# Kernel tuning notes

Measured on AMD Instinct MI355X. Metric: run time of the kernel, lower is better.

The kernel has to match this reference:

```python
import jax, jax.numpy as jnp
import numpy as np

WS = 8          # window size
NH = 8          # num heads
DIM = 256
HD = DIM // NH  # head dim = 32
SCALE = HD ** -0.5
EPS = 1e-5


def _rel_pos_index(ws):
    # deterministic int index buffer, same math as the torch __init__
    coords = jnp.stack(jnp.meshgrid(jnp.arange(ws), jnp.arange(ws), indexing='ij'))  # [2,ws,ws]
    cf = coords.reshape(2, -1)                     # [2, N]
    rel = cf[:, :, None] - cf[:, None, :]          # [2, N, N]
    return (rel[0] + ws - 1) * (2 * ws - 1) + (rel[1] + ws - 1)  # [N, N]


def _ln(h, g, b):
    m = jnp.mean(h, axis=-1, keepdims=True)
    v = jnp.mean((h - m) ** 2, axis=-1, keepdims=True)
    return (h - m) / jnp.sqrt(v + EPS) * g + b


def setup_inputs() -> dict:
    key = jax.random.key(0)
    ks = jax.random.split(key, 16)
    B_, N, D = 4096, WS * WS, DIM
    s = 0.02
    return {
        'x':      jax.random.normal(ks[0], (B_, N, D), jnp.float32),
        # enhanced qkv: Linear(D,2D) -> LN -> GELU -> Linear(2D,3D)
        'w_qkv1': jax.random.normal(ks[1], (D, 2 * D), jnp.float32) * s,
        'b_qkv1': jnp.zeros((2 * D,), jnp.float32),
        'g_qkv':  jnp.ones((2 * D,), jnp.float32),
        'be_qkv': jnp.zeros((2 * D,), jnp.float32),
        'w_qkv2': jax.random.normal(ks[2], (2 * D, 3 * D), jnp.float32) * s,
        'b_qkv2': jnp.zeros((3 * D,), jnp.float32),
        # relative position bias table [(2*WS-1)^2, NH]
        'rpb':    jax.random.normal(ks[3], ((2 * WS - 1) ** 2, NH), jnp.float32) * s,
        # enhanced proj: Linear(D,2D) -> LN -> GELU -> Linear(2D,D)
        'w_p1':   jax.random.normal(ks[4], (D, 2 * D), jnp.float32) * s,
        'b_p1':   jnp.zeros((2 * D,), jnp.float32),
        'g_p':    jnp.ones((2 * D,), jnp.float32),
        'be_p':   jnp.zeros((2 * D,), jnp.float32),
        'w_p2':   jax.random.normal(ks[5], (2 * D, D), jnp.float32) * s,
        'b_p2':   jnp.zeros((D,), jnp.float32),
    }


def reference(x, w_qkv1, b_qkv1, g_qkv, be_qkv, w_qkv2, b_qkv2, rpb,
              w_p1, b_p1, g_p, be_p, w_p2, b_p2):
    B_, N, C = x.shape
    # enhanced QKV chain: Linear -> LayerNorm -> GELU -> Linear
    h = jax.nn.gelu(_ln(x @ w_qkv1 + b_qkv1, g_qkv, be_qkv), approximate=False)
    qkv = h @ w_qkv2 + b_qkv2                              # [B_, N, 3C]
    qkv = qkv.reshape(B_, N, 3, NH, HD).transpose(2, 0, 3, 1, 4)  # [3, B_, H, N, hd]
    q, k, v = qkv[0], qkv[1], qkv[2]
    attn = jnp.einsum('bhnd,bhmd->bhnm', q * SCALE, k)     # [B_, H, N, N]
    idx = _rel_pos_index(WS)                                # [N, N] int
    bias = rpb[idx.reshape(-1)].reshape(N, N, NH).transpose(2, 0, 1)  # [H, N, N]
    attn = jax.nn.softmax(attn + bias[None], axis=-1)
    out = jnp.einsum('bhnm,bhmd->bhnd', attn, v)           # [B_, H, N, hd]
    out = out.transpose(0, 2, 1, 3).reshape(B_, N, C)
    # enhanced proj chain: Linear -> LayerNorm -> GELU -> Linear
    h = jax.nn.gelu(_ln(out @ w_p1 + b_p1, g_p, be_p), approximate=False)
    return h @ w_p2 + b_p2
```

## Files before the change

kernel.cpp:

```cpp
#include <hip/hip_runtime.h>


typedef __bf16 bf16_t;
typedef __bf16 bf16x8 __attribute__((ext_vector_type(8)));
typedef __bf16 bf16x4 __attribute__((ext_vector_type(4)));
typedef float f32x4 __attribute__((ext_vector_type(4)));

__device__ __forceinline__ f32x4 mfma16(bf16x8 a, bf16x8 b, f32x4 acc) {
  return __builtin_amdgcn_mfma_f32_16x16x32_bf16(a, b, acc, 0, 0, 0);
}

#define SWZ(row, byteoff) ((byteoff) ^ (((row) & 7) << 4))

__device__ __forceinline__ float gelu_f(float v) {
  float e = __expf(v * (1.59576912f + 0.07135482f * v * v));
  return v - v * __builtin_amdgcn_rcpf(1.0f + e);
}

__global__ void prep_kernel(const float* __restrict__ w1, const float* __restrict__ w2,
                            const float* __restrict__ wp1, const float* __restrict__ wp2,
                            const float* __restrict__ rpb,
                            bf16_t* __restrict__ w1t, bf16_t* __restrict__ w2t,
                            bf16_t* __restrict__ wp1t, bf16_t* __restrict__ wp2t,
                            float* __restrict__ bt) {
  int i = blockIdx.x * 256 + threadIdx.x;
  if (i < 131072) {
    int k = i & 255, n = i >> 8;
    w1t[i] = (bf16_t)w1[k * 512 + n];
    return;
  }
  i -= 131072;
  if (i < 393216) {
    int k = i & 511, n = i >> 9;
    w2t[i] = (bf16_t)w2[k * 768 + n];
    return;
  }
  i -= 393216;
  if (i < 131072) {
    int k = i & 255, n = i >> 8;
    wp1t[i] = (bf16_t)wp1[k * 512 + n];
    return;
  }
  i -= 131072;
  if (i < 131072) {
    int k = i & 511, n = i >> 9;
    wp2t[i] = (bf16_t)wp2[k * 256 + n];
    return;
  }
  i -= 131072;
  if (i < 32768) {
    int hd = i >> 12, r = (i >> 6) & 63, j = i & 63;
    int idx = ((r >> 3) - (j >> 3) + 7) * 15 + ((r & 7) - (j & 7) + 7);
    bt[i] = rpb[idx * 8 + hd];
  }
}

__device__ __forceinline__ void gemmT_ln_gelu16(
    const char* bsrc, const bf16_t* __restrict__ wt,
    const float* __restrict__ bias, const float* __restrict__ gamma,
    const float* __restrict__ beta,
    char* dst, int flb, float2* part, int wave, int g, int c)
{
  f32x4 acc[2][4] = {};
#pragma unroll
  for (int kt = 0; kt < 8; ++kt) {
    bf16x8 a[2], b[4];
#pragma unroll
    for (int mt = 0; mt < 2; ++mt)
      a[mt] = *(const bf16x8*)(wt + (size_t)(wave * 32 + mt * 16 + c) * 256 + kt * 32 + g * 8);
#pragma unroll
    for (int nt = 0; nt < 4; ++nt) {
      int T = nt * 16 + c;
      b[nt] = *(const bf16x8*)(bsrc + SWZ(T, T * 512 + kt * 64 + g * 16));
    }
#pragma unroll
    for (int mt = 0; mt < 2; ++mt)
#pragma unroll
      for (int nt = 0; nt < 4; ++nt)
        acc[mt][nt] = mfma16(a[mt], b[nt], acc[mt][nt]);
  }
  float s[4] = {0.f, 0.f, 0.f, 0.f}, ss[4] = {0.f, 0.f, 0.f, 0.f};
#pragma unroll
  for (int mt = 0; mt < 2; ++mt) {
    float4 b4 = *(const float4*)(bias + wave * 32 + mt * 16 + g * 4);
#pragma unroll
    for (int nt = 0; nt < 4; ++nt)
#pragma unroll
      for (int r = 0; r < 4; ++r) {
        float v = acc[mt][nt][r] + ((const float*)&b4)[r];
        acc[mt][nt][r] = v;
        s[nt] += v;
        ss[nt] += v * v;
      }
  }
#pragma unroll
  for (int nt = 0; nt < 4; ++nt) {
    float sv = s[nt], ssv = ss[nt];
    sv += __shfl_xor(sv, 16, 64); ssv += __shfl_xor(ssv, 16, 64);
    sv += __shfl_xor(sv, 32, 64); ssv += __shfl_xor(ssv, 32, 64);
    if (g == 0) part[wave * 64 + nt * 16 + c] = make_float2(sv, ssv);
  }
  __syncthreads();
#pragma unroll
  for (int nt = 0; nt < 4; ++nt) {
    float sv = 0.f, ssv = 0.f;
#pragma unroll
    for (int w = 0; w < 16; ++w) {
      float2 p2 = part[w * 64 + nt * 16 + c];
      sv += p2.x; ssv += p2.y;
    }
    float m = sv * (1.f / 512.f);
    float rstd = rsqrtf(ssv * (1.f / 512.f) - m * m + 1e-5f);
#pragma unroll
    for (int mt = 0; mt < 2; ++mt)
#pragma unroll
      for (int r = 0; r < 4; ++r)
        acc[mt][nt][r] = (acc[mt][nt][r] - m) * rstd;
  }
#pragma unroll
  for (int mt = 0; mt < 2; ++mt) {
    float4 g4 = *(const float4*)(gamma + wave * 32 + mt * 16 + g * 4);
    float4 be4 = *(const float4*)(beta + wave * 32 + mt * 16 + g * 4);
    int f0 = flb + mt * 16 + g * 4;
#pragma unroll
    for (int nt = 0; nt < 4; ++nt) {
      int T = nt * 16 + c;
      bf16x4 h4;
#pragma unroll
      for (int r = 0; r < 4; ++r) {
        float v = acc[mt][nt][r] * ((const float*)&g4)[r] + ((const float*)&be4)[r];
        h4[r] = (bf16_t)gelu_f(v);
      }
      *(bf16x4*)(dst + SWZ(T, T * 512 + f0 * 2)) = h4;
    }
  }
}

__global__ __launch_bounds__(1024, 1) void g1qa_kernel(
    const float* __restrict__ x,
    const bf16_t* __restrict__ w1t, const float* __restrict__ b1,
    const float* __restrict__ gamma1, const float* __restrict__ beta1,
    const bf16_t* __restrict__ w2t, const float* __restrict__ b2,
    const float* __restrict__ bt,
    bf16_t* __restrict__ ao)
{
  __shared__ __align__(16) char sm[163840];
  char* rA = sm;
  char* rB = sm + 32768;
  float2* part = (float2*)(sm + 65536);
  const int tid = threadIdx.x;
  const int wave = tid >> 6, lane = tid & 63;
  const int g = lane >> 4, c = lane & 15;
  const int win = blockIdx.x;

  const float* xw = x + (size_t)win * 16384;
#pragma unroll
  for (int it = 0; it < 4; ++it) {
    int e = it * 4096 + tid * 4;
    float4 v = *(const float4*)(xw + e);
    int row = e >> 8, col = e & 255;
    bf16x4 t4;
    t4[0] = (bf16_t)v.x; t4[1] = (bf16_t)v.y; t4[2] = (bf16_t)v.z; t4[3] = (bf16_t)v.w;
    *(bf16x4*)(rA + SWZ(row, row * 512 + col * 2)) = t4;
  }
  __syncthreads();
  gemmT_ln_gelu16(rA, w1t, b1, gamma1, beta1, (wave < 8) ? rB : rA, (wave & 7) * 32,
                  part, wave, g, c);
  __syncthreads();

  const int hh = wave >> 1, mh = wave & 1;
  {
    f32x4 accv[4] = {}, accq[4] = {}, acck[4] = {};
    const bf16_t* wq = w2t + (size_t)(hh * 32 + mh * 16 + c) * 512;
    const bf16_t* wk = wq + (size_t)256 * 512;
    const bf16_t* wv = wq + (size_t)512 * 512;
#pragma unroll
    for (int kt = 0; kt < 16; ++kt) {
      const char* hb = (kt < 8) ? rB : rA;
      const int ko = (kt & 7) * 64 + g * 16;
      bf16x8 av = *(const bf16x8*)(wv + kt * 32 + g * 8);
      bf16x8 aq = *(const bf16x8*)(wq + kt * 32 + g * 8);
      bf16x8 ak = *(const bf16x8*)(wk + kt * 32 + g * 8);
      bf16x8 b[4];
#pragma unroll
      for (int nt = 0; nt < 4; ++nt) {
        int T = nt * 16 + c;
        b[nt] = *(const bf16x8*)(hb + SWZ(T, T * 512 + ko));
      }
#pragma unroll
      for (int nt = 0; nt < 4; ++nt) {
        accv[nt] = mfma16(av, b[nt], accv[nt]);
        accq[nt] = mfma16(aq, b[nt], accq[nt]);
        acck[nt] = mfma16(ak, b[nt], acck[nt]);
      }
    }
    float4 bv4 = *(const float4*)(b2 + 512 + hh * 32 + mh * 16 + g * 4);
    float4 bq4 = *(const float4*)(b2 + hh * 32 + mh * 16 + g * 4);
    float4 bk4 = *(const float4*)(b2 + 256 + hh * 32 + mh * 16 + g * 4);
    char* qb = sm + 65536 + hh * 8192;
    char* vs = sm + 131072 + hh * 4096;
    const int d0 = mh * 16 + g * 4;
#pragma unroll
    for (int nt = 0; nt < 4; ++nt) {
      int T = nt * 16 + c;
      bf16x4 q4, k4;
#pragma unroll
      for (int r = 0; r < 4; ++r) {
        q4[r] = (bf16_t)((accq[nt][r] + ((const float*)&bq4)[r]) * 0.17677669529663687f);
        k4[r] = (bf16_t)(acck[nt][r] + ((const float*)&bk4)[r]);
      }
      *(bf16x4*)(qb + SWZ(T, T * 64 + d0 * 2)) = q4;
      *(bf16x4*)(qb + 4096 + SWZ(T, T * 64 + d0 * 2)) = k4;
#pragma unroll
      for (int r = 0; r < 4; ++r) {
        int d = d0 + r;
        *(bf16_t*)(vs + SWZ(d, d * 128 + T * 2)) =
            (bf16_t)(accv[nt][r] + ((const float*)&bv4)[r]);
      }
    }
  }
  __syncthreads();

  const int h8 = wave & 7, rowbase = (wave >> 3) * 32;
  char* qb = sm + 65536 + h8 * 8192;
  char* vslot = sm + 131072 + h8 * 4096;
  const float* btab = bt + h8 * 4096;

  bf16x8 aq[2], bk[4];
#pragma unroll
  for (int mt = 0; mt < 2; ++mt) {
    int t = rowbase + mt * 16 + c;
    aq[mt] = *(const bf16x8*)(qb + SWZ(t, t * 64 + g * 16));
  }
#pragma unroll
  for (int nt = 0; nt < 4; ++nt) {
    int t = nt * 16 + c;
    bk[nt] = *(const bf16x8*)(qb + 4096 + SWZ(t, t * 64 + g * 16));
  }
  float p[2][4][4];
#pragma unroll
  for (int mt = 0; mt < 2; ++mt)
#pragma unroll
    for (int nt = 0; nt < 4; ++nt) {
      f32x4 z = {0.f, 0.f, 0.f, 0.f};
      f32x4 s4 = mfma16(aq[mt], bk[nt], z);
#pragma unroll
      for (int r = 0; r < 4; ++r) {
        int i = rowbase + mt * 16 + g * 4 + r, j = nt * 16 + c;
        p[mt][nt][r] = s4[r] + btab[i * 64 + j];
      }
    }
#pragma unroll
  for (int mt = 0; mt < 2; ++mt)
#pragma unroll
    for (int r = 0; r < 4; ++r) {
      float mx = fmaxf(fmaxf(p[mt][0][r], p[mt][1][r]), fmaxf(p[mt][2][r], p[mt][3][r]));
#pragma unroll
      for (int m = 1; m < 16; m <<= 1) mx = fmaxf(mx, __shfl_xor(mx, m, 64));
      float sum = 0.f;
#pragma unroll
      for (int nt = 0; nt < 4; ++nt) {
        float e = __expf(p[mt][nt][r] - mx);
        p[mt][nt][r] = e; sum += e;
      }
#pragma unroll
      for (int m = 1; m < 16; m <<= 1) sum += __shfl_xor(sum, m, 64);
      float rinv = 1.f / sum;
#pragma unroll
      for (int nt = 0; nt < 4; ++nt) p[mt][nt][r] *= rinv;
    }
  __syncthreads();

#pragma unroll
  for (int mt = 0; mt < 2; ++mt)
#pragma unroll
    for (int nt = 0; nt < 4; ++nt)
#pragma unroll
      for (int r = 0; r < 4; ++r) {
        int i = rowbase + mt * 16 + g * 4 + r, j = nt * 16 + c;
        *(bf16_t*)(qb + SWZ(i, i * 128 + j * 2)) = (bf16_t)p[mt][nt][r];
      }
  asm volatile("s_waitcnt lgkmcnt(0)" ::: "memory");
  f32x4 oacc[2][2] = {};
#pragma unroll
  for (int kp = 0; kp < 2; ++kp) {
    bf16x8 ap[2], bv[2];
#pragma unroll
    for (int mt = 0; mt < 2; ++mt) {
      int t = rowbase + mt * 16 + c;
      ap[mt] = *(const bf16x8*)(qb + SWZ(t, t * 128 + kp * 64 + g * 16));
    }
#pragma unroll
    for (int nt = 0; nt < 2; ++nt) {
      int d = nt * 16 + c;
      bv[nt] = *(const bf16x8*)(vslot + SWZ(d, d * 128 + kp * 64 + g * 16));
    }
#pragma unroll
    for (int mt = 0; mt < 2; ++mt)
#pragma unroll
      for (int nt = 0; nt < 2; ++nt)
        oacc[mt][nt] = mfma16(ap[mt], bv[nt], oacc[mt][nt]);
  }
#pragma unroll
  for (int mt = 0; mt < 2; ++mt)
#pragma unroll
    for (int nt = 0; nt < 2; ++nt)
#pragma unroll
      for (int r = 0; r < 4; ++r) {
        int T = rowbase + mt * 16 + g * 4 + r;
        ao[(size_t)(win * 64 + T) * 256 + h8 * 32 + nt * 16 + c] = (bf16_t)oacc[mt][nt][r];
      }
}

__global__ __launch_bounds__(1024, 1) void g3g4_kernel(
    const bf16_t* __restrict__ ao,
    const bf16_t* __restrict__ wp1t, const float* __restrict__ bp1,
    const float* __restrict__ gp, const float* __restrict__ bep,
    const bf16_t* __restrict__ wp2t, const float* __restrict__ bp2,
    float* __restrict__ out)
{
  __shared__ __align__(16) char sm[73728];
  char* rA = sm;
  char* rB = sm + 32768;
  float2* part = (float2*)(sm + 65536);
  const int tid = threadIdx.x;
  const int wave = tid >> 6, lane = tid & 63;
  const int g = lane >> 4, c = lane & 15;
  const int win = blockIdx.x;

  const bf16_t* aow = ao + (size_t)win * 16384;
#pragma unroll
  for (int it = 0; it < 2; ++it) {
    int e = it * 8192 + tid * 8;
    bf16x8 v = *(const bf16x8*)(aow + e);
    int row = e >> 8, col = e & 255;
    *(bf16x8*)(rA + SWZ(row, row * 512 + col * 2)) = v;
  }
  __syncthreads();
  gemmT_ln_gelu16(rA, wp1t, bp1, gp, bep, (wave < 8) ? rB : rA, (wave & 7) * 32,
                  part, wave, g, c);
  __syncthreads();

  {
    const int f0 = (wave & 7) * 32, t0 = (wave >> 3) * 32;
    f32x4 acc[2][2] = {};
#pragma unroll
    for (int kt = 0; kt < 16; ++kt) {
      const char* hb = (kt < 8) ? rB : rA;
      const int ko = (kt & 7) * 64 + g * 16;
      bf16x8 a[2], b[2];
#pragma unroll
      for (int mt = 0; mt < 2; ++mt)
        a[mt] = *(const bf16x8*)(wp2t + (size_t)(f0 + mt * 16 + c) * 512 + kt * 32 + g * 8);
#pragma unroll
      for (int nt = 0; nt < 2; ++nt) {
        int T = t0 + nt * 16 + c;
        b[nt] = *(const bf16x8*)(hb + SWZ(T, T * 512 + ko));
      }
#pragma unroll
      for (int mt = 0; mt < 2; ++mt)
#pragma unroll
        for (int nt = 0; nt < 2; ++nt)
          acc[mt][nt] = mfma16(a[mt], b[nt], acc[mt][nt]);
    }
    float* ow = out + (size_t)win * 16384;
#pragma unroll
    for (int mt = 0; mt < 2; ++mt) {
      float4 b4 = *(const float4*)(bp2 + f0 + mt * 16 + g * 4);
#pragma unroll
      for (int nt = 0; nt < 2; ++nt) {
        int T = t0 + nt * 16 + c;
        f32x4 o4;
#pragma unroll
        for (int r = 0; r < 4; ++r) o4[r] = acc[mt][nt][r] + ((const float*)&b4)[r];
        *(f32x4*)(ow + T * 256 + f0 + mt * 16 + g * 4) = o4;
      }
    }
  }
}

extern "C" void kernel_launch(void* const* d_in, const int* in_sizes, int n_in,
                              void* d_out, int out_size, void* d_ws, size_t ws_size,
                              hipStream_t stream) {
  const float* x   = (const float*)d_in[0];
  const float* w1  = (const float*)d_in[1];
  const float* b1  = (const float*)d_in[2];
  const float* g1  = (const float*)d_in[3];
  const float* be1 = (const float*)d_in[4];
  const float* w2  = (const float*)d_in[5];
  const float* b2  = (const float*)d_in[6];
  const float* rpb = (const float*)d_in[7];
  const float* wp1 = (const float*)d_in[8];
  const float* bp1 = (const float*)d_in[9];
  const float* gp  = (const float*)d_in[10];
  const float* bep = (const float*)d_in[11];
  const float* wp2 = (const float*)d_in[12];
  const float* bp2 = (const float*)d_in[13];
  float* out = (float*)d_out;
  char* ws = (char*)d_ws;
  bf16_t* w1t  = (bf16_t*)(ws + 0);
  bf16_t* w2t  = (bf16_t*)(ws + 262144);
  bf16_t* wp1t = (bf16_t*)(ws + 1048576);
  bf16_t* wp2t = (bf16_t*)(ws + 1310720);
  float*  bt   = (float*)(ws + 1572864);
  bf16_t* ao   = (bf16_t*)(ws + 2097152);

  prep_kernel<<<3200, 256, 0, stream>>>(w1, w2, wp1, wp2, rpb,
                                        w1t, w2t, wp1t, wp2t, bt);

  g1qa_kernel<<<4096, 1024, 0, stream>>>(x, w1t, b1, g1, be1, w2t, b2, bt, ao);
  g3g4_kernel<<<4096, 1024, 0, stream>>>(ao, wp1t, bp1, gp, bep, wp2t, bp2, out);
}
```

Measured before the change: 1.209 ms.

## Split projection chain into 32-token blocks of 512 threads, two blocks per CU

The fused proj kernel (Linear→LN→GELU→Linear) now processes 32 tokens per block with 512 threads instead of a 64-token window with 1024 threads, launching twice as many blocks. Launch bounds allow two blocks per CU and shared memory drops from 72KB to 50KB. The first GEMM and the LayerNorm are inlined in place of the shared helper. The aim is better occupancy and overlap between blocks. The cost is that each block reloads the full wp1t and wp2t weights for half as many tokens, which doubles weight traffic from L2.

Result: no change. 1.216 ms (+0.6%).

```diff
diff --git a/kernel.cpp b/kernel.cpp
--- a/kernel.cpp
+++ b/kernel.cpp
@@ -312,68 +312,141 @@
       }
 }
 
-__global__ __launch_bounds__(1024, 1) void g3g4_kernel(
+__global__ __launch_bounds__(512, 2) void g3g4h_kernel(
     const bf16_t* __restrict__ ao,
     const bf16_t* __restrict__ wp1t, const float* __restrict__ bp1,
     const float* __restrict__ gp, const float* __restrict__ bep,
     const bf16_t* __restrict__ wp2t, const float* __restrict__ bp2,
     float* __restrict__ out)
 {
-  __shared__ __align__(16) char sm[73728];
-  char* rA = sm;
-  char* rB = sm + 32768;
-  float2* part = (float2*)(sm + 65536);
+  __shared__ __align__(16) char sm[51200];
+  char* aoT = sm;
+  char* h2 = sm + 16384;
+  float2* part = (float2*)(sm + 49152);
   const int tid = threadIdx.x;
   const int wave = tid >> 6, lane = tid & 63;
   const int g = lane >> 4, c = lane & 15;
-  const int win = blockIdx.x;
-
-  const bf16_t* aow = ao + (size_t)win * 16384;
+  const size_t tokbase = (size_t)blockIdx.x * 32;
+
+  const bf16_t* aow = ao + tokbase * 256;
 #pragma unroll
   for (int it = 0; it < 2; ++it) {
-    int e = it * 8192 + tid * 8;
+    int e = it * 4096 + tid * 8;
     bf16x8 v = *(const bf16x8*)(aow + e);
     int row = e >> 8, col = e & 255;
-    *(bf16x8*)(rA + SWZ(row, row * 512 + col * 2)) = v;
-  }
-  __syncthreads();
-  gemmT_ln_gelu16(rA, wp1t, bp1, gp, bep, (wave < 8) ? rB : rA, (wave & 7) * 32,
-                  part, wave, g, c);
+    *(bf16x8*)(aoT + SWZ(row, row * 512 + col * 2)) = v;
+  }
   __syncthreads();
 
   {
-    const int f0 = (wave & 7) * 32, t0 = (wave >> 3) * 32;
-    f32x4 acc[2][2] = {};
-#pragma unroll
-    for (int kt = 0; kt < 16; ++kt) {
-      const char* hb = (kt < 8) ? rB : rA;
-      const int ko = (kt & 7) * 64 + g * 16;
-      bf16x8 a[2], b[2];
-#pragma unroll
-      for (int mt = 0; mt < 2; ++mt)
-        a[mt] = *(const bf16x8*)(wp2t + (size_t)(f0 + mt * 16 + c) * 512 + kt * 32 + g * 8);
+    f32x4 acc[4][2] = {};
+    const int f0 = wave * 64;
+#pragma unroll
+    for (int kt = 0; kt < 8; ++kt) {
+      bf16x8 a[4], b[2];
+#pragma unroll
+      for (int mt = 0; mt < 4; ++mt)
+        a[mt] = *(const bf16x8*)(wp1t + (size_t)(f0 + mt * 16 + c) * 256 + kt * 32 + g * 8);
 #pragma unroll
       for (int nt = 0; nt < 2; ++nt) {
-        int T = t0 + nt * 16 + c;
-        b[nt] = *(const bf16x8*)(hb + SWZ(T, T * 512 + ko));
-      }
-#pragma unroll
-      for (int mt = 0; mt < 2; ++mt)
+        int T = nt * 16 + c;
+        b[nt] = *(const bf16x8*)(aoT + SWZ(T, T * 512 + kt * 64 + g * 16));
+      }
+#pragma unroll
+      for (int mt = 0; mt < 4; ++mt)
 #pragma unroll
         for (int nt = 0; nt < 2; ++nt)
           acc[mt][nt] = mfma16(a[mt], b[nt], acc[mt][nt]);
     }
-    float* ow = out + (size_t)win * 16384;
+    float s[2] = {0.f, 0.f}, ss[2] = {0.f, 0.f};
+#pragma unroll
+    for (int mt = 0; mt < 4; ++mt) {
+      float4 b4 = *(const float4*)(bp1 + f0 + mt * 16 + g * 4);
+#pragma unroll
+      for (int nt = 0; nt < 2; ++nt)
+#pragma unroll
+        for (int r = 0; r < 4; ++r) {
+          float v = acc[mt][nt][r] + ((const float*)&b4)[r];
+          acc[mt][nt][r] = v;
+          s[nt] += v;
+          ss[nt] += v * v;
+        }
+    }
+#pragma unroll
+    for (int nt = 0; nt < 2; ++nt) {
+      float sv = s[nt], ssv = ss[nt];
+      sv += __shfl_xor(sv, 16, 64); ssv += __shfl_xor(ssv, 16, 64);
+      sv += __shfl_xor(sv, 32, 64); ssv += __shfl_xor(ssv, 32, 64);
+      if (g == 0) part[wave * 32 + nt * 16 + c] = make_float2(sv, ssv);
+    }
+    __syncthreads();
+#pragma unroll
+    for (int nt = 0; nt < 2; ++nt) {
+      float sv = 0.f, ssv = 0.f;
+#pragma unroll
+      for (int w = 0; w < 8; ++w) {
+        float2 p2 = part[w * 32 + nt * 16 + c];
+        sv += p2.x; ssv += p2.y;
+      }
+      float m = sv * (1.f / 512.f);
+      float rstd = rsqrtf(ssv * (1.f / 512.f) - m * m + 1e-5f);
+#pragma unroll
+      for (int mt = 0; mt < 4; ++mt)
+#pragma unroll
+        for (int r = 0; r < 4; ++r)
+          acc[mt][nt][r] = (acc[mt][nt][r] - m) * rstd;
+    }
+#pragma unroll
+    for (int mt = 0; mt < 4; ++mt) {
+      float4 g4 = *(const float4*)(gp + f0 + mt * 16 + g * 4);
+      float4 be4 = *(const float4*)(bep + f0 + mt * 16 + g * 4);
+      int fb = (f0 + mt * 16 + g * 4) * 2;
+#pragma unroll
+      for (int nt = 0; nt < 2; ++nt) {
+        int T = nt * 16 + c;
+        bf16x4 h4;
+#pragma unroll
+        for (int r = 0; r < 4; ++r) {
+          float v = acc[mt][nt][r] * ((const float*)&g4)[r] + ((const float*)&be4)[r];
+          h4[r] = (bf16_t)gelu_f(v);
+        }
+        *(bf16x4*)(h2 + SWZ(T, T * 1024 + fb)) = h4;
+      }
+    }
+  }
+  __syncthreads();
+
+  {
+    const int o0 = wave * 32;
+    f32x4 acc[2][2] = {};
+#pragma unroll
+    for (int kt = 0; kt < 16; ++kt) {
+      bf16x8 a[2], b[2];
+#pragma unroll
+      for (int mt = 0; mt < 2; ++mt)
+        a[mt] = *(const bf16x8*)(wp2t + (size_t)(o0 + mt * 16 + c) * 512 + kt * 32 + g * 8);
+#pragma unroll
+      for (int nt = 0; nt < 2; ++nt) {
+        int T = nt * 16 + c;
+        b[nt] = *(const bf16x8*)(h2 + SWZ(T, T * 1024 + kt * 64 + g * 16));
+      }
+#pragma unroll
+      for (int mt = 0; mt < 2; ++mt)
+#pragma unroll
+        for (int nt = 0; nt < 2; ++nt)
+          acc[mt][nt] = mfma16(a[mt], b[nt], acc[mt][nt]);
+    }
+    float* ow = out + tokbase * 256;
 #pragma unroll
     for (int mt = 0; mt < 2; ++mt) {
-      float4 b4 = *(const float4*)(bp2 + f0 + mt * 16 + g * 4);
+      float4 b4 = *(const float4*)(bp2 + o0 + mt * 16 + g * 4);
 #pragma unroll
       for (int nt = 0; nt < 2; ++nt) {
-        int T = t0 + nt * 16 + c;
+        int T = nt * 16 + c;
         f32x4 o4;
 #pragma unroll
         for (int r = 0; r < 4; ++r) o4[r] = acc[mt][nt][r] + ((const float*)&b4)[r];
-        *(f32x4*)(ow + T * 256 + f0 + mt * 16 + g * 4) = o4;
+        *(f32x4*)(ow + T * 256 + o0 + mt * 16 + g * 4) = o4;
       }
     }
   }
@@ -409,5 +482,5 @@
                                         w1t, w2t, wp1t, wp2t, bt);
 
   g1qa_kernel<<<4096, 1024, 0, stream>>>(x, w1t, b1, g1, be1, w2t, b2, bt, ao);
-  g3g4_kernel<<<4096, 1024, 0, stream>>>(ao, wp1t, bp1, gp, bep, wp2t, bp2, out);
-}
+  g3g4h_kernel<<<8192, 512, 0, stream>>>(ao, wp1t, bp1, gp, bep, wp2t, bp2, out);
+}
```
